# Optimization experiments

Hardware: AMD Instinct MI355X
Metric: run time of the kernel (lower is better)

## Reference

```python
import jax, jax.numpy as jnp
import numpy as np

BS = 32
WIDTH = 4
DEPTH = 5
D_MODEL = 1024
MAX_LEN = 2048
MAX_D_TREE_PARAM = 64


def _build_tree_positions(bs, width, depth):
    """One-hot path encodings for a complete `width`-ary tree of height `depth`.
    Replicates TreePosEnc_for_one_sent's integer traversal: node v (1-indexed)
    has parent (v-1)//width and child-index (v-1)%width; path ids are collected
    from the node up to the root, level 0 = closest to the node.
    Returns float32 [bs, n_nodes, depth*width]."""
    n_nodes = sum(width ** l for l in range(1, depth + 1))  # non-root nodes
    pos = np.zeros((n_nodes, depth * width), dtype=np.float32)
    for v in range(1, n_nodes + 1):
        u, level = v, 0
        while u != 0:
            pid = (u - 1) % width
            pos[v - 1, level * width + pid] = 1.0
            u = (u - 1) // width
            level += 1
    return np.broadcast_to(pos[None], (bs, n_nodes, depth * width)).copy()


def setup_inputs() -> dict:
    key = jax.random.key(0)
    k_p, _ = jax.random.split(key)
    # matches init_weights(): uniform(0.7, 0.999)
    p = jax.random.uniform(k_p, (MAX_D_TREE_PARAM,), dtype=jnp.float32,
                           minval=0.7, maxval=0.999)
    positions = jnp.asarray(_build_tree_positions(BS, WIDTH, DEPTH))
    return {
        "p": p,
        "positions": positions,   # [bs, n_nodes, depth*width], one-hot paths
        "width": WIDTH,
        "depth": DEPTH,
        "n_dim": D_MODEL,
        "max_len": MAX_LEN,
    }


def reference(p, positions, width, depth, n_dim, max_len):
    bs, n_nodes, _ = positions.shape
    n_feat = n_dim // (width * depth)
    # build_weights: tanh-parameterized geometric decay over tree levels
    tp = jnp.tanh(p[:n_feat])                                   # [f]
    levels = jnp.arange(depth, dtype=positions.dtype)           # [d]
    tree_norm = jnp.sqrt((1.0 - jnp.square(tp)) * n_dim / 2.0)  # [f]
    w_df = (tp[None, :] ** levels[:, None]) * tree_norm[None, :]        # [d, f]
    tree_weights = jnp.broadcast_to(w_df[:, None, :], (depth, width, n_feat))
    tree_weights = tree_weights.reshape(depth * width, n_feat)          # [d*w, f]
    # treeify_positions: outer product over the per-level one-hot ids
    treeified = positions[..., None] * tree_weights                     # [bs, n, d*w, f]
    treeified = treeified.reshape(bs, n_nodes, depth * width * n_feat)
    # pad feature dim up to n_dim, then sos + tail padding along sequence
    feat_pad = jnp.zeros((bs, n_nodes, n_dim - depth * width * n_feat),
                         dtype=treeified.dtype)
    enc = jnp.concatenate([treeified, feat_pad], axis=-1)               # [bs, n, n_dim]
    sos = jnp.zeros((bs, 1, n_dim), dtype=enc.dtype)
    tail = jnp.zeros((bs, max_len - n_nodes - 1, n_dim), dtype=enc.dtype)
    return jnp.concatenate([sos, enc, tail], axis=1)                    # [bs, max_len, n_dim]
```

## Files before the change

kernel.cpp:

```cpp
#include <hip/hip_runtime.h>
#include <hip/hip_bf16.h>

constexpr int kBS     = 32;
constexpr int kMaxLen = 2048;
constexpr int kNNodes = 1364;
constexpr int kNDim   = 1024;
constexpr int kDepth  = 5;
constexpr int kWidth  = 4;
constexpr int kNFeat  = kNDim / (kDepth * kWidth);
constexpr int kDW     = kDepth * kWidth;
constexpr int kUsed   = kDW * kNFeat;


__global__ __launch_bounds__(256) void tree_pos_enc_kernel(
    const float* __restrict__ p,
    const float* __restrict__ positions,
    float* __restrict__ out,
    int total_chunks)
{
    __shared__ float s_w[kDepth * kNFeat];
    {
        int t = threadIdx.x;
        if (t < kDepth * kNFeat) {
            int d = t / kNFeat;
            int f = t - d * kNFeat;
            float tp   = tanhf(p[f]);
            float norm = sqrtf((1.0f - tp * tp) * (float)kNDim * 0.5f);
            float w = norm;
            #pragma unroll
            for (int i = 0; i < kDepth - 1; ++i)
                if (i < d) w *= tp;
            s_w[t] = w;
        }
    }
    __syncthreads();

    const int stride = gridDim.x * blockDim.x;
    for (int idx = blockIdx.x * blockDim.x + threadIdx.x;
         idx < total_chunks; idx += stride) {
        const int row = idx >> 8;
        const int c0  = (idx & 255) << 2;
        const int b   = row >> 11;
        const int seq = row & (kMaxLen - 1);

        float vals[4] = {0.0f, 0.0f, 0.0f, 0.0f};
        if (!(seq == 0 || seq > kNNodes || c0 >= kUsed)) {
            const int node = seq - 1;
            const float* posrow =
                positions + ((size_t)b * kNNodes + (size_t)node) * kDW;
            #pragma unroll
            for (int j = 0; j < 4; ++j) {
                const int c = c0 + j;
                const int dw = c / kNFeat;
                const int f  = c - dw * kNFeat;
                const float pv = posrow[dw];
                vals[j] = pv * s_w[(dw >> 2) * kNFeat + f];
            }
        }

        *reinterpret_cast<float4*>(out + (size_t)idx * 4) =
            make_float4(vals[0], vals[1], vals[2], vals[3]);
    }
}

extern "C" void kernel_launch(void* const* d_in, const int* in_sizes, int n_in,
                              void* d_out, int out_size, void* d_ws, size_t ws_size,
                              hipStream_t stream) {
    const float* p         = (const float*)d_in[0];
    const float* positions = (const float*)d_in[1];
    float* out             = (float*)d_out;

    const int total_chunks = out_size / 4;
    const int threads = 256;
    const int blocks  = 2048;

    tree_pos_enc_kernel<<<blocks, threads, 0, stream>>>(p, positions, out,
                                                        total_chunks);
}
```

Baseline: 50.33 us.

## Assign one block per sequence row and loop over batch, hoisting per-column weights

Replaces the grid-stride loop over flat output chunks with one block per sequence position, where each thread handles a fixed 4-column chunk and iterates over all 32 batch entries. The per-column divisions and shared-memory weight lookups are computed once per thread instead of once per output element, and padding rows take an all-zero store path. This lowers index arithmetic and redundant weight loads, but each thread now does 32 strided stores, and the grid is fixed at 2048 blocks regardless of output size.

```diff
diff --git a/kernel.cpp b/kernel.cpp
--- a/kernel.cpp
+++ b/kernel.cpp
@@ -15,17 +15,16 @@
 __global__ __launch_bounds__(256) void tree_pos_enc_kernel(
     const float* __restrict__ p,
     const float* __restrict__ positions,
-    float* __restrict__ out,
-    int total_chunks)
+    float* __restrict__ out)
 {
     __shared__ float s_w[kDepth * kNFeat];
     {
-        int t = threadIdx.x;
+        const int t = threadIdx.x;
         if (t < kDepth * kNFeat) {
-            int d = t / kNFeat;
-            int f = t - d * kNFeat;
-            float tp   = tanhf(p[f]);
-            float norm = sqrtf((1.0f - tp * tp) * (float)kNDim * 0.5f);
+            const int d = t / kNFeat;
+            const int f = t - d * kNFeat;
+            const float tp   = tanhf(p[f]);
+            const float norm = sqrtf((1.0f - tp * tp) * (float)kNDim * 0.5f);
             float w = norm;
             #pragma unroll
             for (int i = 0; i < kDepth - 1; ++i)
@@ -35,31 +34,44 @@
     }
     __syncthreads();
 
-    const int stride = gridDim.x * blockDim.x;
-    for (int idx = blockIdx.x * blockDim.x + threadIdx.x;
-         idx < total_chunks; idx += stride) {
-        const int row = idx >> 8;
-        const int c0  = (idx & 255) << 2;
-        const int b   = row >> 11;
-        const int seq = row & (kMaxLen - 1);
+    const int seq = blockIdx.x;
+    const int c0  = threadIdx.x << 2;
+    float* optr = out + (size_t)seq * kNDim + c0;
+    constexpr size_t kBStride = (size_t)kMaxLen * kNDim;
 
-        float vals[4] = {0.0f, 0.0f, 0.0f, 0.0f};
-        if (!(seq == 0 || seq > kNNodes || c0 >= kUsed)) {
-            const int node = seq - 1;
-            const float* posrow =
-                positions + ((size_t)b * kNNodes + (size_t)node) * kDW;
-            #pragma unroll
-            for (int j = 0; j < 4; ++j) {
-                const int c = c0 + j;
-                const int dw = c / kNFeat;
-                const int f  = c - dw * kNFeat;
-                const float pv = posrow[dw];
-                vals[j] = pv * s_w[(dw >> 2) * kNFeat + f];
-            }
-        }
+    if (seq == 0 || seq > kNNodes) {
+        const float4 z = make_float4(0.f, 0.f, 0.f, 0.f);
+        #pragma unroll 8
+        for (int b = 0; b < kBS; ++b)
+            *reinterpret_cast<float4*>(optr + (size_t)b * kBStride) = z;
+        return;
+    }
 
-        *reinterpret_cast<float4*>(out + (size_t)idx * 4) =
-            make_float4(vals[0], vals[1], vals[2], vals[3]);
+    int   dwj[4];
+    float wj[4];
+    bool  used[4];
+    #pragma unroll
+    for (int j = 0; j < 4; ++j) {
+        const int c = c0 + j;
+        used[j] = (c < kUsed);
+        const int dw = used[j] ? (c / kNFeat) : 0;
+        const int f  = c - dw * kNFeat;
+        dwj[j] = dw;
+        wj[j]  = used[j] ? s_w[(dw >> 2) * kNFeat + f] : 0.0f;
+    }
+
+    const int node = seq - 1;
+    const float* posbase = positions + (size_t)node * kDW;
+
+    #pragma unroll 4
+    for (int b = 0; b < kBS; ++b) {
+        const float* posrow = posbase + (size_t)b * (kNNodes * kDW);
+        float4 v;
+        v.x = used[0] ? posrow[dwj[0]] * wj[0] : 0.0f;
+        v.y = used[1] ? posrow[dwj[1]] * wj[1] : 0.0f;
+        v.z = used[2] ? posrow[dwj[2]] * wj[2] : 0.0f;
+        v.w = used[3] ? posrow[dwj[3]] * wj[3] : 0.0f;
+        *reinterpret_cast<float4*>(optr + (size_t)b * kBStride) = v;
     }
 }
 
@@ -70,10 +82,5 @@
     const float* positions = (const float*)d_in[1];
     float* out             = (float*)d_out;
 
-    const int total_chunks = out_size / 4;
-    const int threads = 256;
-    const int blocks  = 2048;
-
-    tree_pos_enc_kernel<<<blocks, threads, 0, stream>>>(p, positions, out,
-                                                        total_chunks);
+    tree_pos_enc_kernel<<<kMaxLen, 256, 0, stream>>>(p, positions, out);
 }
```

After: 66.32 us. 1.32x slower.
